# Kernel tuning notes

Hardware: AMD Instinct MI355X
Metric: run time of the kernel (lower is better)

## Reference

```python
import jax, jax.numpy as jnp
import numpy as np

B, P, K, L, F, KS, NCLS = 8, 4096, 20, 10, 32, 5, 40
N = B * P


def setup_inputs() -> dict:
    key = jax.random.key(0)
    k = jax.random.split(key, 5)
    return {
        "pos": jax.random.normal(k[0], (N, 3), jnp.float32),
        "Wsp": jax.random.normal(k[1], (KS ** 3, F), jnp.float32) * 0.1,
        "root": jax.random.normal(k[2], (F,), jnp.float32) * 0.1,
        "bias": jnp.zeros((F,), jnp.float32),
        "gamma": jnp.ones((F,), jnp.float32),
        "beta": jnp.zeros((F,), jnp.float32),
        "W1": jax.random.normal(k[3], (F, 256), jnp.float32) * 0.1,
        "b1": jnp.zeros((256,), jnp.float32),
        "W2": jax.random.normal(k[4], (256, NCLS), jnp.float32) * 0.1,
        "b2": jnp.zeros((NCLS,), jnp.float32),
    }


def _knn(pos):
    # per-graph brute-force knn (loop=False), neighbors sorted by distance
    pts = pos.reshape(B, P, 3)

    def one(p):
        d = jnp.sum((p[:, None, :] - p[None, :, :]) ** 2, -1)  # (P,P)
        d = d.at[jnp.arange(P), jnp.arange(P)].set(jnp.inf)
        return jax.lax.top_k(-d, K)[1]

    nbr = jax.vmap(one)(pts) + (jnp.arange(B) * P)[:, None, None]
    return nbr.reshape(N, K)


def _eig3(A):
    # power iteration with deflation (nr_iterations=5) on batched 3x3 symmetric mats
    def pi(M):
        v = jnp.full((M.shape[0], 3), np.float32(3.0 ** -0.5))
        for _ in range(5):
            v = jnp.einsum("nij,nj->ni", M, v)
            v = v / (jnp.linalg.norm(v, axis=-1, keepdims=True) + 1e-12)
        lam = jnp.einsum("ni,nij,nj->n", v, M, v)
        return lam, v

    l1, v1 = pi(A)
    _, v2 = pi(A - l1[:, None, None] * v1[:, :, None] * v1[:, None, :])
    v3 = jnp.cross(v1, v2)
    v3 = v3 / (jnp.linalg.norm(v3, axis=-1, keepdims=True) + 1e-12)
    return jnp.stack([v1, v2, v3], axis=1)  # rows = eigenvectors, V[:,2] = normal


def reference(pos, Wsp, root, bias, gamma, beta, W1, b1, W2, b2):
    nbr = _knn(pos)                               # (N,K)
    clusters = pos[nbr] - pos[:, None, :]         # (N,K,3) neighbor - center
    cov = jnp.einsum("nmc,nmd->ncd", clusters[:, :L], clusters[:, :L])
    V = _eig3(cov)                                # (N,3,3)
    dirc = jnp.einsum("nkc,ndc->nkd", clusters, V)  # clusters @ V^T
    signs = jnp.sign(dirc[:, :, 2].sum(1))
    dirc = dirc.at[:, :, 2].multiply(signs[:, None])
    max_abs = jnp.max(jnp.abs(dirc).reshape(N, -1), 1)
    dirc = dirc / max_abs[:, None, None] * 0.5 + 0.5  # pseudo coords in [0,1]

    # SplineConv, degree=1, open splines, dim=3, in_channels=1 (x=ones)
    v = dirc * (KS - 1)
    f = jnp.floor(v)
    frac = v - f
    fi = f.astype(jnp.int32)
    bits = jnp.array([[(s >> 2) & 1, (s >> 1) & 1, s & 1] for s in range(8)], jnp.int32)
    idx = jnp.clip(fi[:, :, None, :] + bits[None, None, :, :], 0, KS - 1)  # (N,K,8,3)
    wgt = jnp.where(bits[None, None] == 1, frac[:, :, None, :], 1.0 - frac[:, :, None, :])
    basis = wgt.prod(-1)                                          # (N,K,8)
    flat = (idx[..., 0] * KS + idx[..., 1]) * KS + idx[..., 2]    # (N,K,8)
    msg = jnp.einsum("nks,nksf->nf", basis, Wsp[flat]) / K        # mean aggregation
    node = msg + root + bias                                      # root weight on x=1

    # BatchNorm1d (training-mode batch stats, eps=1e-5)
    mu = node.mean(0)
    var = ((node - mu) ** 2).mean(0)
    xb = gamma * (node - mu) / jnp.sqrt(var + 1e-5) + beta

    out3 = xb[:, :, None] * V[:, 2][:, None, :]   # (N,F,3) scale normal direction
    y = jax.nn.sigmoid(out3)
    ys = y.reshape(-1, P, F).mean(1)              # (3B,F) as in torch .view
    y1 = jax.nn.elu(ys @ W1 + b1)
    return jax.nn.log_softmax(y1 @ W2 + b2, axis=1)
```

## Files before the change

### kernel.cpp

```cpp
#include <hip/hip_runtime.h>
#include <hip/hip_bf16.h>
#include <math.h>

#define BGR 8
#define PP 4096
#define NPTS 32768
#define KNN 20
#define LCOV 10
#define FF 32
#define KS 5
#define NCLS 40
#define NGROUP 24
#define GROUPLEN 131072

#define SPLIT 8
#define CHUNK (PP / SPLIT)
#define PTSBLK 128
#define KTHR 1024
#define NSLOT (KNN + 1)
#define MPAD NSLOT
#define SENT 0xFFFFFFFFu
#define SCELLS 4096
#define SCAP 12

__device__ inline unsigned umn(unsigned a, unsigned b) { return a < b ? a : b; }
__device__ inline unsigned umx(unsigned a, unsigned b) { return a > b ? a : b; }

__device__ inline void mat3vec(const float M[9], const float v[3], float w[3]) {
    w[0] = M[0] * v[0] + M[1] * v[1] + M[2] * v[2];
    w[1] = M[3] * v[0] + M[4] * v[1] + M[5] * v[2];
    w[2] = M[6] * v[0] + M[7] * v[1] + M[8] * v[2];
}

__device__ inline float pi3(const float M[9], float v[3]) {
    v[0] = v[1] = v[2] = 0.57735026918962576f;
#pragma unroll
    for (int it = 0; it < 5; ++it) {
        float w[3];
        mat3vec(M, v, w);
        float nrm = sqrtf(w[0] * w[0] + w[1] * w[1] + w[2] * w[2]) + 1e-12f;
        v[0] = w[0] / nrm;
        v[1] = w[1] / nrm;
        v[2] = w[2] / nrm;
    }
    float w[3];
    mat3vec(M, v, w);
    return v[0] * w[0] + v[1] * w[1] + v[2] * w[2];
}

__global__ __launch_bounds__(KTHR, 4) void knn_kernel(
    const float* __restrict__ pos, unsigned short* __restrict__ nbr16,
    float* __restrict__ Rbuf, float* __restrict__ v3out) {
    __shared__ float smem[4 * PP];
    __shared__ unsigned short mOrig[PP];
    __shared__ unsigned samp[PTSBLK * 24];
    __shared__ float Tseed[PTSBLK];
    __shared__ unsigned scr[KTHR / 64][SCAP][64];
    float* tx = smem;
    float* ty = smem + PP;
    float* tz = smem + 2 * PP;
    float* tw = smem + 3 * PP;
    unsigned short* lnbr = (unsigned short*)(smem + 3 * PP + 2816);

    int b = blockIdx.x >> 5;
    int blkInGraph = blockIdx.x & 31;
    const float* gp = pos + (size_t)b * PP * 3;
    int tid = threadIdx.x;
    int lane = tid & 63;
    int wid = tid >> 6;

    {
        unsigned* cnt = (unsigned*)smem;
        unsigned short* cellOf = (unsigned short*)(smem + 4096);
        unsigned* tsum = (unsigned*)(smem + 6144);
        for (int i = tid; i < SCELLS; i += KTHR) cnt[i] = 0u;
        __syncthreads();
        for (int i = tid; i < PP; i += KTHR) {
            float x = gp[i * 3 + 0];
            float y = gp[i * 3 + 1];
            float z = gp[i * 3 + 2];
            int cx = min(max((int)floorf((x + 4.0f) * 2.0f), 0), 15);
            int cy = min(max((int)floorf((y + 4.0f) * 2.0f), 0), 15);
            int cz = min(max((int)floorf((z + 4.0f) * 2.0f), 0), 15);
            unsigned m = 0;
#pragma unroll
            for (int bb = 0; bb < 4; ++bb)
                m |= (((unsigned)(cx >> bb) & 1u) << (3 * bb + 2)) |
                     (((unsigned)(cy >> bb) & 1u) << (3 * bb + 1)) |
                     (((unsigned)(cz >> bb) & 1u) << (3 * bb + 0));
            cellOf[i] = (unsigned short)m;
            atomicAdd(&cnt[m], 1u);
        }
        __syncthreads();
        unsigned c0 = cnt[4 * tid + 0];
        unsigned c1 = cnt[4 * tid + 1];
        unsigned c2 = cnt[4 * tid + 2];
        unsigned c3 = cnt[4 * tid + 3];
        unsigned local = c0 + c1 + c2 + c3;
        tsum[tid] = local;
        __syncthreads();
        for (int off = 1; off < 1024; off <<= 1) {
            unsigned v = (tid >= off) ? tsum[tid - off] : 0u;
            __syncthreads();
            tsum[tid] += v;
            __syncthreads();
        }
        unsigned base = tsum[tid] - local;
        cnt[4 * tid + 0] = base;
        cnt[4 * tid + 1] = base + c0;
        cnt[4 * tid + 2] = base + c0 + c1;
        cnt[4 * tid + 3] = base + c0 + c1 + c2;
        __syncthreads();
        for (int i = tid; i < PP; i += KTHR) {
            unsigned dst = atomicAdd(&cnt[cellOf[i]], 1u);
            mOrig[dst] = (unsigned short)i;
        }
    }
    __syncthreads();

    for (int i = tid; i < PP; i += KTHR) {
        float x = gp[i * 3 + 0];
        float y = gp[i * 3 + 1];
        float z = gp[i * 3 + 2];
        tx[i] = -2.0f * x;
        ty[i] = -2.0f * y;
        tz[i] = -2.0f * z;
        tw[i] = x * x + y * y + z * z;
    }
    __syncthreads();

    int eighth = tid >> 7;
    int pt = tid & (PTSBLK - 1);
    int qSlot = blkInGraph * PTSBLK + pt;
    int li = mOrig[qSlot];
    float px = -0.5f * tx[li];
    float py = -0.5f * ty[li];
    float pz = -0.5f * tz[li];
    float p2 = tw[li];
    int jbeg = eighth * CHUNK;

    {
        unsigned s0 = SENT, s1 = SENT, s2 = SENT;
#pragma unroll 4
        for (int c = 0; c < 32; ++c) {
            int base = jbeg + c * 16;
            float4 xv = *(const float4*)(tx + base);
            float4 yv = *(const float4*)(ty + base);
            float4 zv = *(const float4*)(tz + base);
            float4 wv = *(const float4*)(tw + base);
            float xa[4] = {xv.x, xv.y, xv.z, xv.w};
            float ya[4] = {yv.x, yv.y, yv.z, yv.w};
            float za[4] = {zv.x, zv.y, zv.z, zv.w};
            float wa[4] = {wv.x, wv.y, wv.z, wv.w};
#pragma unroll
            for (int u = 0; u < 4; ++u) {
                float dh = fmaf(px, xa[u], fmaf(py, ya[u], fmaf(pz, za[u], wa[u])));
                float d = fmaxf(dh + p2, 0.0f);
                unsigned key = (__float_as_uint(d) & 0xFFFFF000u)
                               | (unsigned)(base + u);
                if (base + u == li) key = SENT;
                unsigned t0 = umn(key, s0); key = umx(key, s0); s0 = t0;
                t0 = umn(key, s1); key = umx(key, s1); s1 = t0;
                s2 = umn(key, s2);
            }
        }
        unsigned* sdst = &samp[pt * 24 + eighth * 3];
        sdst[0] = s0; sdst[1] = s1; sdst[2] = s2;
    }
    __syncthreads();
    if (tid < PTSBLK) {
        unsigned g0 = 0, g1 = 0, g2 = 0, g3 = 0;
        const unsigned* ss = &samp[tid * 24];
#pragma unroll
        for (int i = 0; i < 24; ++i) {
            unsigned k = ss[i], a;
            a = umx(k, g0); k = umn(k, g0); g0 = a;
            a = umx(k, g1); k = umn(k, g1); g1 = a;
            a = umx(k, g2); k = umn(k, g2); g2 = a;
            g3 = umx(k, g3);
        }
        Tseed[tid] = __uint_as_float((g3 & 0xFFFFF000u) + 0x2000u);
    }
    __syncthreads();
    float seed_hat = Tseed[pt] - p2;

    unsigned bd[NSLOT];
#pragma unroll
    for (int k = 0; k < NSLOT; k++) bd[k] = SENT;
    float worst_hat = seed_hat;

    unsigned* scrW = &scr[wid][0][0];
    unsigned cnt = 0;

    auto drain = [&]() {
#pragma unroll
        for (int s = 0; s < SCAP; ++s) {
            if (!__any((int)cnt > s)) break;
            unsigned k = (s < (int)cnt) ? scrW[s * 64 + lane] : SENT;
#pragma unroll
            for (int i = 0; i < NSLOT; i++) {
                unsigned lo = umn(k, bd[i]);
                k = umx(k, bd[i]);
                bd[i] = lo;
            }
        }
        cnt = 0;
        unsigned wb = bd[NSLOT - 1];
        float nw = (wb == SENT) ? INFINITY
                                : __uint_as_float(wb & 0xFFFFF000u) - p2;
        worst_hat = fminf(nw, seed_hat);
    };

    for (int jj = jbeg; jj < jbeg + CHUNK; jj += 8) {
        float4 xv0 = *(const float4*)(tx + jj);
        float4 yv0 = *(const float4*)(ty + jj);
        float4 zv0 = *(const float4*)(tz + jj);
        float4 wv0 = *(const float4*)(tw + jj);
        float4 xv1 = *(const float4*)(tx + jj + 4);
        float4 yv1 = *(const float4*)(ty + jj + 4);
        float4 zv1 = *(const float4*)(tz + jj + 4);
        float4 wv1 = *(const float4*)(tw + jj + 4);
        float xa[8] = {xv0.x, xv0.y, xv0.z, xv0.w, xv1.x, xv1.y, xv1.z, xv1.w};
        float ya[8] = {yv0.x, yv0.y, yv0.z, yv0.w, yv1.x, yv1.y, yv1.z, yv1.w};
        float za[8] = {zv0.x, zv0.y, zv0.z, zv0.w, zv1.x, zv1.y, zv1.z, zv1.w};
        float wa[8] = {wv0.x, wv0.y, wv0.z, wv0.w, wv1.x, wv1.y, wv1.z, wv1.w};
#pragma unroll
        for (int u = 0; u < 8; u++) {
            float dh = fmaf(px, xa[u], fmaf(py, ya[u], fmaf(pz, za[u], wa[u])));
            if (dh < worst_hat) {
                float d = fmaxf(dh + p2, 0.0f);
                scrW[cnt * 64 + lane] = (__float_as_uint(d) & 0xFFFFF000u)
                                        | (unsigned)(jj + u);
                cnt++;
            }
        }
        if (__any(cnt >= 4u)) drain();
    }
    drain();

    __syncthreads();
    unsigned* mk = (unsigned*)smem;
    for (int h = 0; h < 2; h++) {
        if ((pt >> 6) == h) {
            int lpt = pt & 63;
#pragma unroll
            for (int k = 0; k < NSLOT; k++)
                mk[(eighth * 64 + lpt) * MPAD + k] = bd[k];
        }
        __syncthreads();
        if (tid < 64) {
            int p = tid;
            const unsigned* base = &mk[p * MPAD];
            int cur[SPLIT];
#pragma unroll
            for (int q = 0; q < SPLIT; q++) cur[q] = 0;
            int lpt2 = h * 64 + p;
            int gi = b * PP + (int)mOrig[blkInGraph * PTSBLK + lpt2];
#pragma unroll
            for (int t = 0; t < NSLOT; t++) {
                unsigned v[SPLIT];
#pragma unroll
                for (int q = 0; q < SPLIT; q++)
                    v[q] = base[q * 64 * MPAD + cur[q]];
                unsigned m = v[0];
#pragma unroll
                for (int q = 1; q < SPLIT; q++) m = umn(m, v[q]);
                if (t > 0) {
                    int local = (int)(m & 0xFFFu);
                    nbr16[(size_t)gi * KNN + (t - 1)] = (unsigned short)local;
                    lnbr[lpt2 * KNN + (t - 1)] = (unsigned short)local;
                }
#pragma unroll
                for (int q = 0; q < SPLIT; q++) cur[q] += (v[q] == m);
            }
        }
        __syncthreads();
    }

    for (int i = tid; i < PP; i += KTHR) {
        tx[i] = gp[i * 3 + 0];
        ty[i] = gp[i * 3 + 1];
        tz[i] = gp[i * 3 + 2];
    }
    __syncthreads();

    if (tid < PTSBLK) {
        int lp = tid;
        int ng = mOrig[blkInGraph * PTSBLK + lp];
        int n = b * PP + ng;
        float qx = tx[ng], qy = ty[ng], qz = tz[ng];
        const unsigned short* ln = &lnbr[lp * KNN];

        float m00 = 0.f, m01 = 0.f, m02 = 0.f, m11 = 0.f, m12 = 0.f, m22 = 0.f;
#pragma unroll
        for (int k = 0; k < LCOV; k++) {
            int id = ln[k];
            float cx = tx[id] - qx;
            float cy = ty[id] - qy;
            float cz = tz[id] - qz;
            m00 += cx * cx; m01 += cx * cy; m02 += cx * cz;
            m11 += cy * cy; m12 += cy * cz; m22 += cz * cz;
        }
        float M[9] = {m00, m01, m02, m01, m11, m12, m02, m12, m22};

        float v1[3], v2[3], v3[3];
        float l1 = pi3(M, v1);
        float M2[9];
#pragma unroll
        for (int c = 0; c < 3; c++)
#pragma unroll
            for (int d = 0; d < 3; d++)
                M2[c * 3 + d] = M[c * 3 + d] - l1 * v1[c] * v1[d];
        pi3(M2, v2);
        v3[0] = v1[1] * v2[2] - v1[2] * v2[1];
        v3[1] = v1[2] * v2[0] - v1[0] * v2[2];
        v3[2] = v1[0] * v2[1] - v1[1] * v2[0];
        {
            float nrm = sqrtf(v3[0] * v3[0] + v3[1] * v3[1] + v3[2] * v3[2]) + 1e-12f;
            v3[0] /= nrm; v3[1] /= nrm; v3[2] /= nrm;
        }

        float ssum = 0.f, mx = 0.f;
#pragma unroll
        for (int k = 0; k < KNN; k++) {
            int id = ln[k];
            float cx = tx[id] - qx;
            float cy = ty[id] - qy;
            float cz = tz[id] - qz;
            float d0 = cx * v1[0] + cy * v1[1] + cz * v1[2];
            float d1 = cx * v2[0] + cy * v2[1] + cz * v2[2];
            float d2 = cx * v3[0] + cy * v3[1] + cz * v3[2];
            ssum += d2;
            mx = fmaxf(mx, fabsf(d0));
            mx = fmaxf(mx, fabsf(d1));
            mx = fmaxf(mx, fabsf(d2));
        }
        float sgn = (ssum > 0.f) ? 1.f : ((ssum < 0.f) ? -1.f : 0.f);

        float sc = 2.0f / mx;
        float* R = Rbuf + (size_t)n * 12;
        R[0] = v1[0] * sc;  R[1] = v1[1] * sc;  R[2] = v1[2] * sc;
        R[3] = v2[0] * sc;  R[4] = v2[1] * sc;  R[5] = v2[2] * sc;
        float s2 = sgn * sc;
        R[6] = v3[0] * s2;  R[7] = v3[1] * s2;  R[8] = v3[2] * s2;
        R[9] = 0.f; R[10] = 0.f; R[11] = 0.f;

        v3out[n * 3 + 0] = v3[0];
        v3out[n * 3 + 1] = v3[1];
        v3out[n * 3 + 2] = v3[2];
    }
}

#define NPB 16
#define SPLBLKS (NPTS / NPB)
__global__ __launch_bounds__(512) void spline_kernel(
    const float* __restrict__ pos, const unsigned short* __restrict__ nbr16,
    const float* __restrict__ Rbuf, const float* __restrict__ Wsp,
    const float* __restrict__ root, const float* __restrict__ bias,
    float* __restrict__ node, float* __restrict__ sums_part) {
    __shared__ float wbuf[NPB * KNN * 8];

    int tid = threadIdx.x;
    if (tid < NPB * KNN) {
        int pt = tid / KNN;
        int k = tid - pt * KNN;
        int n = blockIdx.x * NPB + pt;
        const float4* Rv = (const float4*)(Rbuf + (size_t)n * 12);
        float4 r0 = Rv[0], r1 = Rv[1], r2 = Rv[2];
        float px = pos[n * 3 + 0], py = pos[n * 3 + 1], pz = pos[n * 3 + 2];
        int id = (n & ~(PP - 1)) | (int)nbr16[(size_t)n * KNN + k];
        float cxx = pos[id * 3 + 0] - px;
        float cyy = pos[id * 3 + 1] - py;
        float czz = pos[id * 3 + 2] - pz;
        float v0 = fmaf(cxx, r0.x, fmaf(cyy, r0.y, fmaf(czz, r0.z, 2.0f)));
        float v1 = fmaf(cxx, r0.w, fmaf(cyy, r1.x, fmaf(czz, r1.y, 2.0f)));
        float v2 = fmaf(cxx, r1.z, fmaf(cyy, r1.w, fmaf(czz, r2.x, 2.0f)));
        float f0 = floorf(v0), f1 = floorf(v1), f2 = floorf(v2);
        float fr0 = v0 - f0, fr1 = v1 - f1, fr2 = v2 - f2;
        int fi0 = (int)f0, fi1 = (int)f1, fi2 = (int)f2;
        float* wdst = &wbuf[(pt * KNN + k) * 8];
#pragma unroll
        for (int s = 0; s < 8; s++) {
            int b0 = (s >> 2) & 1, b1 = (s >> 1) & 1, b2s = s & 1;
            int i0 = min(max(fi0 + b0, 0), KS - 1);
            int i1 = min(max(fi1 + b1, 0), KS - 1);
            int i2 = min(max(fi2 + b2s, 0), KS - 1);
            float w = (b0 ? fr0 : 1.f - fr0) * (b1 ? fr1 : 1.f - fr1) *
                      (b2s ? fr2 : 1.f - fr2);
            unsigned flat = (unsigned)((i0 * KS + i1) * KS + i2);
            wdst[s] = __uint_as_float((__float_as_uint(w) & ~127u) | flat);
        }
    }
    __syncthreads();

    int pt = tid >> 5;
    int f = tid & 31;
    const float* wrow = &wbuf[pt * (KNN * 8)];
    float acc = 0.f;
#pragma unroll
    for (int k = 0; k < KNN; k++) {
        float4 wa = *(const float4*)&wrow[k * 8];
        float4 wb = *(const float4*)&wrow[k * 8 + 4];
        float wv[8] = {wa.x, wa.y, wa.z, wa.w, wb.x, wb.y, wb.z, wb.w};
#pragma unroll
        for (int s = 0; s < 8; s++) {
            unsigned u = __float_as_uint(wv[s]) & 127u;
            acc = fmaf(wv[s], Wsp[u * FF + f], acc);
        }
    }
    int n = blockIdx.x * NPB + pt;
    float val = acc * (1.0f / KNN) + root[f] + bias[f];
    node[(size_t)n * FF + f] = val;

    __syncthreads();
    wbuf[tid] = val;
    wbuf[512 + tid] = val * val;
    __syncthreads();
    if (tid < 64) {
        int ff = tid & 31;
        int off = (tid >> 5) * 512;
        float s = 0.f;
#pragma unroll
        for (int p = 0; p < NPB; p++) s += wbuf[off + p * 32 + ff];
        sums_part[(size_t)blockIdx.x * 64 + tid] = s;
    }
}

__global__ __launch_bounds__(256) void stats_kernel(
    const float* __restrict__ sums_part, float* __restrict__ sums_accum) {
    int c = blockIdx.x;
    __shared__ float red[256];
    float s = 0.f;
    for (int r = threadIdx.x; r < SPLBLKS; r += 256)
        s += sums_part[(size_t)r * 64 + c];
    red[threadIdx.x] = s;
    __syncthreads();
    for (int off = 128; off > 0; off >>= 1) {
        if (threadIdx.x < off) red[threadIdx.x] += red[threadIdx.x + off];
        __syncthreads();
    }
    if (threadIdx.x == 0) sums_accum[c] = red[0];
}

#define YSPLIT 32
#define YCHUNK (GROUPLEN / YSPLIT)
__global__ __launch_bounds__(256) void ys_kernel(
    const float* __restrict__ node, const float* __restrict__ v3,
    const float* __restrict__ sums_accum, const float* __restrict__ gamma,
    const float* __restrict__ beta, float* __restrict__ ys_part) {
    __shared__ float sa[FF], sb[FF];
    if (threadIdx.x < FF) {
        int f = threadIdx.x;
        float mu = sums_accum[f] * (1.0f / NPTS);
        float var = sums_accum[FF + f] * (1.0f / NPTS) - mu * mu;
        float inv = 1.0f / sqrtf(var + 1e-5f);
        sa[f] = gamma[f] * inv;
        sb[f] = beta[f] - gamma[f] * inv * mu;
    }
    __syncthreads();

    int g = blockIdx.x >> 5;
    int sub = blockIdx.x & 31;
    int t0 = g * GROUPLEN + sub * YCHUNK + threadIdx.x;
    int n = t0 / 96;
    int r0 = t0 - n * 96;
    int rj[3], fj[3], cj[3], dj[3];
    rj[0] = r0;
    rj[1] = (r0 + 64) % 96;
    rj[2] = (r0 + 32) % 96;
#pragma unroll
    for (int j = 0; j < 3; j++) {
        fj[j] = rj[j] / 3;
        cj[j] = rj[j] - fj[j] * 3;
        dj[j] = (rj[j] >= 32) ? 3 : 2;
    }
    float Sa0 = sa[fj[0]], Sb0 = sb[fj[0]];
    float Sa1 = sa[fj[1]], Sb1 = sb[fj[1]];
    float Sa2 = sa[fj[2]], Sb2 = sb[fj[2]];
    int nf = n * FF;
    int n3 = n * 3;

    float acc = 0.f;
#pragma unroll 1
    for (int tr = 0; tr < 5; tr++) {
        {
            float xb = fmaf(Sa0, node[nf + fj[0]], Sb0);
            float val = xb * v3[n3 + cj[0]];
            acc += 1.0f / (1.0f + __expf(-val));
            nf += dj[0] * FF; n3 += dj[0] * 3;
        }
        {
            float xb = fmaf(Sa1, node[nf + fj[1]], Sb1);
            float val = xb * v3[n3 + cj[1]];
            acc += 1.0f / (1.0f + __expf(-val));
            nf += dj[1] * FF; n3 += dj[1] * 3;
        }
        {
            float xb = fmaf(Sa2, node[nf + fj[2]], Sb2);
            float val = xb * v3[n3 + cj[2]];
            acc += 1.0f / (1.0f + __expf(-val));
            nf += dj[2] * FF; n3 += dj[2] * 3;
        }
    }
    {
        float xb = fmaf(Sa0, node[nf + fj[0]], Sb0);
        float val = xb * v3[n3 + cj[0]];
        acc += 1.0f / (1.0f + __expf(-val));
    }

    __shared__ float red[256];
    red[threadIdx.x] = acc;
    __syncthreads();
    if (threadIdx.x < FF) {
        float s = 0.f;
        for (int t = threadIdx.x; t < 256; t += FF) s += red[t];
        ys_part[(sub * NGROUP + g) * FF + threadIdx.x] = s * (1.0f / PP);
    }
}

__global__ __launch_bounds__(256) void head_kernel(
    const float* __restrict__ ys_part, const float* __restrict__ W1,
    const float* __restrict__ b1, const float* __restrict__ W2,
    const float* __restrict__ b2, float* __restrict__ out) {
    int g = blockIdx.x;
    __shared__ float syr[FF];
    __shared__ float h[256];
    __shared__ float logits[NCLS];
    __shared__ float mstat[2];
    if (threadIdx.x < FF) {
        float s = 0.f;
#pragma unroll
        for (int sub = 0; sub < YSPLIT; sub++)
            s += ys_part[(sub * NGROUP + g) * FF + threadIdx.x];
        syr[threadIdx.x] = s;
    }
    __syncthreads();
    int j = threadIdx.x;
    float acc = b1[j];
#pragma unroll
    for (int f = 0; f < FF; f++) acc += syr[f] * W1[f * 256 + j];
    h[j] = acc > 0.f ? acc : expm1f(acc);
    __syncthreads();
    if (j < NCLS) {
        float l = b2[j];
        for (int q = 0; q < 256; q++) l += h[q] * W2[q * NCLS + j];
        logits[j] = l;
    }
    __syncthreads();
    if (j == 0) {
        float m = -INFINITY;
        for (int o = 0; o < NCLS; o++) m = fmaxf(m, logits[o]);
        float s = 0.f;
        for (int o = 0; o < NCLS; o++) s += expf(logits[o] - m);
        mstat[0] = m;
        mstat[1] = logf(s);
    }
    __syncthreads();
    if (j < NCLS) out[g * NCLS + j] = logits[j] - mstat[0] - mstat[1];
}

extern "C" void kernel_launch(void* const* d_in, const int* in_sizes, int n_in,
                              void* d_out, int out_size, void* d_ws, size_t ws_size,
                              hipStream_t stream) {
    const float* pos   = (const float*)d_in[0];
    const float* Wsp   = (const float*)d_in[1];
    const float* root  = (const float*)d_in[2];
    const float* bias  = (const float*)d_in[3];
    const float* gamma = (const float*)d_in[4];
    const float* beta  = (const float*)d_in[5];
    const float* W1    = (const float*)d_in[6];
    const float* b1    = (const float*)d_in[7];
    const float* W2    = (const float*)d_in[8];
    const float* b2    = (const float*)d_in[9];
    float* out = (float*)d_out;

    char* ws = (char*)d_ws;
    unsigned short* nbr16 = (unsigned short*)(ws);
    float* sums_part = (float*)(ws + 1310720);
    float* ys_part   = (float*)(ws + 1835008);
    float* sums_accum = (float*)(ws + 1933312);
    float* node = (float*)(ws + 2621440);
    float* v3   = (float*)(ws + 6815744);
    float* Rbuf = (float*)(ws + 7212288);

    knn_kernel<<<256, KTHR, 0, stream>>>(pos, nbr16, Rbuf, v3);
    spline_kernel<<<SPLBLKS, 512, 0, stream>>>(pos, nbr16, Rbuf, Wsp, root,
                                               bias, node, sums_part);
    stats_kernel<<<64, 256, 0, stream>>>(sums_part, sums_accum);
    ys_kernel<<<NGROUP * YSPLIT, 256, 0, stream>>>(node, v3, sums_accum, gamma,
                                                   beta, ys_part);
    head_kernel<<<NGROUP, 256, 0, stream>>>(ys_part, W1, b1, W2, b2, out);
}
```

Baseline: 192.8 us.

## Fuse spline convolution and partial batch-norm sums into the knn kernel

Moves the spline basis computation, the Wsp gather-accumulate and the per-block BN partial sums into the end of knn_kernel. Neighbor indices and rotation rows stay in shared memory (lnbr, samp, scr), so the nbr16 and Rbuf global round trips and one launch go away. The cost is that the spline work now runs on only 256 large blocks instead of 2048 small ones, which reduces parallelism for that phase and adds extra barriers and shared-memory reuse inside the already heavy knn kernel.

```diff
diff --git a/kernel.cpp b/kernel.cpp
--- a/kernel.cpp
+++ b/kernel.cpp
@@ -22,6 +22,7 @@
 #define SENT 0xFFFFFFFFu
 #define SCELLS 4096
 #define SCAP 12
+#define KBLKS 256
 
 __device__ inline unsigned umn(unsigned a, unsigned b) { return a < b ? a : b; }
 __device__ inline unsigned umx(unsigned a, unsigned b) { return a > b ? a : b; }
@@ -49,8 +50,10 @@
 }
 
 __global__ __launch_bounds__(KTHR, 4) void knn_kernel(
-    const float* __restrict__ pos, unsigned short* __restrict__ nbr16,
-    float* __restrict__ Rbuf, float* __restrict__ v3out) {
+    const float* __restrict__ pos, const float* __restrict__ Wsp,
+    const float* __restrict__ root, const float* __restrict__ bias,
+    float* __restrict__ node, float* __restrict__ sums_part,
+    float* __restrict__ v3out) {
     __shared__ float smem[4 * PP];
     __shared__ unsigned short mOrig[PP];
     __shared__ unsigned samp[PTSBLK * 24];
@@ -255,7 +258,6 @@
 #pragma unroll
             for (int q = 0; q < SPLIT; q++) cur[q] = 0;
             int lpt2 = h * 64 + p;
-            int gi = b * PP + (int)mOrig[blkInGraph * PTSBLK + lpt2];
 #pragma unroll
             for (int t = 0; t < NSLOT; t++) {
                 unsigned v[SPLIT];
@@ -266,9 +268,7 @@
 #pragma unroll
                 for (int q = 1; q < SPLIT; q++) m = umn(m, v[q]);
                 if (t > 0) {
-                    int local = (int)(m & 0xFFFu);
-                    nbr16[(size_t)gi * KNN + (t - 1)] = (unsigned short)local;
-                    lnbr[lpt2 * KNN + (t - 1)] = (unsigned short)local;
+                    lnbr[lpt2 * KNN + (t - 1)] = (unsigned short)(m & 0xFFFu);
                 }
 #pragma unroll
                 for (int q = 0; q < SPLIT; q++) cur[q] += (v[q] == m);
@@ -338,91 +338,91 @@
         float sgn = (ssum > 0.f) ? 1.f : ((ssum < 0.f) ? -1.f : 0.f);
 
         float sc = 2.0f / mx;
-        float* R = Rbuf + (size_t)n * 12;
-        R[0] = v1[0] * sc;  R[1] = v1[1] * sc;  R[2] = v1[2] * sc;
-        R[3] = v2[0] * sc;  R[4] = v2[1] * sc;  R[5] = v2[2] * sc;
-        float s2 = sgn * sc;
-        R[6] = v3[0] * s2;  R[7] = v3[1] * s2;  R[8] = v3[2] * s2;
-        R[9] = 0.f; R[10] = 0.f; R[11] = 0.f;
+        float* rrow = (float*)samp + lp * 12;
+        rrow[0] = v1[0] * sc;  rrow[1] = v1[1] * sc;  rrow[2] = v1[2] * sc;
+        rrow[3] = v2[0] * sc;  rrow[4] = v2[1] * sc;  rrow[5] = v2[2] * sc;
+        float s2g = sgn * sc;
+        rrow[6] = v3[0] * s2g; rrow[7] = v3[1] * s2g; rrow[8] = v3[2] * s2g;
 
         v3out[n * 3 + 0] = v3[0];
         v3out[n * 3 + 1] = v3[1];
         v3out[n * 3 + 2] = v3[2];
     }
-}
-
-#define NPB 16
-#define SPLBLKS (NPTS / NPB)
-__global__ __launch_bounds__(512) void spline_kernel(
-    const float* __restrict__ pos, const unsigned short* __restrict__ nbr16,
-    const float* __restrict__ Rbuf, const float* __restrict__ Wsp,
-    const float* __restrict__ root, const float* __restrict__ bias,
-    float* __restrict__ node, float* __restrict__ sums_part) {
-    __shared__ float wbuf[NPB * KNN * 8];
-
-    int tid = threadIdx.x;
-    if (tid < NPB * KNN) {
-        int pt = tid / KNN;
-        int k = tid - pt * KNN;
-        int n = blockIdx.x * NPB + pt;
-        const float4* Rv = (const float4*)(Rbuf + (size_t)n * 12);
-        float4 r0 = Rv[0], r1 = Rv[1], r2 = Rv[2];
-        float px = pos[n * 3 + 0], py = pos[n * 3 + 1], pz = pos[n * 3 + 2];
-        int id = (n & ~(PP - 1)) | (int)nbr16[(size_t)n * KNN + k];
-        float cxx = pos[id * 3 + 0] - px;
-        float cyy = pos[id * 3 + 1] - py;
-        float czz = pos[id * 3 + 2] - pz;
-        float v0 = fmaf(cxx, r0.x, fmaf(cyy, r0.y, fmaf(czz, r0.z, 2.0f)));
-        float v1 = fmaf(cxx, r0.w, fmaf(cyy, r1.x, fmaf(czz, r1.y, 2.0f)));
-        float v2 = fmaf(cxx, r1.z, fmaf(cyy, r1.w, fmaf(czz, r2.x, 2.0f)));
-        float f0 = floorf(v0), f1 = floorf(v1), f2 = floorf(v2);
-        float fr0 = v0 - f0, fr1 = v1 - f1, fr2 = v2 - f2;
-        int fi0 = (int)f0, fi1 = (int)f1, fi2 = (int)f2;
-        float* wdst = &wbuf[(pt * KNN + k) * 8];
-#pragma unroll
-        for (int s = 0; s < 8; s++) {
-            int b0 = (s >> 2) & 1, b1 = (s >> 1) & 1, b2s = s & 1;
-            int i0 = min(max(fi0 + b0, 0), KS - 1);
-            int i1 = min(max(fi1 + b1, 0), KS - 1);
-            int i2 = min(max(fi2 + b2s, 0), KS - 1);
-            float w = (b0 ? fr0 : 1.f - fr0) * (b1 ? fr1 : 1.f - fr1) *
-                      (b2s ? fr2 : 1.f - fr2);
-            unsigned flat = (unsigned)((i0 * KS + i1) * KS + i2);
-            wdst[s] = __uint_as_float((__float_as_uint(w) & ~127u) | flat);
-        }
-    }
-    __syncthreads();
-
-    int pt = tid >> 5;
-    int f = tid & 31;
-    const float* wrow = &wbuf[pt * (KNN * 8)];
-    float acc = 0.f;
-#pragma unroll
-    for (int k = 0; k < KNN; k++) {
-        float4 wa = *(const float4*)&wrow[k * 8];
-        float4 wb = *(const float4*)&wrow[k * 8 + 4];
-        float wv[8] = {wa.x, wa.y, wa.z, wa.w, wb.x, wb.y, wb.z, wb.w};
-#pragma unroll
-        for (int s = 0; s < 8; s++) {
-            unsigned u = __float_as_uint(wv[s]) & 127u;
-            acc = fmaf(wv[s], Wsp[u * FF + f], acc);
-        }
-    }
-    int n = blockIdx.x * NPB + pt;
-    float val = acc * (1.0f / KNN) + root[f] + bias[f];
-    node[(size_t)n * FF + f] = val;
-
-    __syncthreads();
-    wbuf[tid] = val;
-    wbuf[512 + tid] = val * val;
-    __syncthreads();
-    if (tid < 64) {
-        int ff = tid & 31;
-        int off = (tid >> 5) * 512;
-        float s = 0.f;
-#pragma unroll
-        for (int p = 0; p < NPB; p++) s += wbuf[off + p * 32 + ff];
-        sums_part[(size_t)blockIdx.x * 64 + tid] = s;
+    __syncthreads();
+
+    {
+        float* wb = (float*)scr;
+        const float* sampF = (const float*)samp;
+        for (int i = tid; i < PTSBLK * KNN; i += KTHR) {
+            int lp = i / KNN;
+            int k = i - lp * KNN;
+            int ng = mOrig[blkInGraph * PTSBLK + lp];
+            float qx = tx[ng], qy = ty[ng], qz = tz[ng];
+            int id = lnbr[lp * KNN + k];
+            float cxx = tx[id] - qx;
+            float cyy = ty[id] - qy;
+            float czz = tz[id] - qz;
+            const float* r = &sampF[lp * 12];
+            float v0 = fmaf(cxx, r[0], fmaf(cyy, r[1], fmaf(czz, r[2], 2.0f)));
+            float v1 = fmaf(cxx, r[3], fmaf(cyy, r[4], fmaf(czz, r[5], 2.0f)));
+            float v2 = fmaf(cxx, r[6], fmaf(cyy, r[7], fmaf(czz, r[8], 2.0f)));
+            float f0 = floorf(v0), f1 = floorf(v1), f2 = floorf(v2);
+            float fr0 = v0 - f0, fr1 = v1 - f1, fr2 = v2 - f2;
+            int fi0 = (int)f0, fi1 = (int)f1, fi2 = (int)f2;
+            float* wdst = &wb[i * 8];
+#pragma unroll
+            for (int s = 0; s < 8; s++) {
+                int b0 = (s >> 2) & 1, b1 = (s >> 1) & 1, b2s = s & 1;
+                int i0 = min(max(fi0 + b0, 0), KS - 1);
+                int i1 = min(max(fi1 + b1, 0), KS - 1);
+                int i2 = min(max(fi2 + b2s, 0), KS - 1);
+                float w = (b0 ? fr0 : 1.f - fr0) * (b1 ? fr1 : 1.f - fr1) *
+                          (b2s ? fr2 : 1.f - fr2);
+                unsigned flat = (unsigned)((i0 * KS + i1) * KS + i2);
+                wdst[s] = __uint_as_float((__float_as_uint(w) & ~127u) | flat);
+            }
+        }
+    }
+    __syncthreads();
+
+    {
+        const float* wb = (const float*)scr;
+        float bn1 = 0.f, bn2 = 0.f;
+        int f = tid & 31;
+#pragma unroll
+        for (int it = 0; it < 4; ++it) {
+            int lp = (tid >> 5) + 32 * it;
+            const float* wrow = &wb[(lp * KNN) * 8];
+            float acc = 0.f;
+#pragma unroll
+            for (int k = 0; k < KNN; k++) {
+                float4 wa = *(const float4*)&wrow[k * 8];
+                float4 wb4 = *(const float4*)&wrow[k * 8 + 4];
+                float wv[8] = {wa.x, wa.y, wa.z, wa.w, wb4.x, wb4.y, wb4.z, wb4.w};
+#pragma unroll
+                for (int s = 0; s < 8; s++) {
+                    unsigned u = __float_as_uint(wv[s]) & 127u;
+                    acc = fmaf(wv[s], Wsp[u * FF + f], acc);
+                }
+            }
+            float val = acc * (1.0f / KNN) + root[f] + bias[f];
+            int ng = mOrig[blkInGraph * PTSBLK + lp];
+            node[((size_t)b * PP + ng) * FF + f] = val;
+            bn1 += val;
+            bn2 += val * val;
+        }
+        float* redF = (float*)samp;
+        redF[tid] = bn1;
+        redF[1024 + tid] = bn2;
+        __syncthreads();
+        if (tid < 64) {
+            int ff = tid & 31;
+            int off = (tid >> 5) * 1024;
+            float s = 0.f;
+#pragma unroll
+            for (int g = 0; g < 32; ++g) s += redF[off + (g << 5) + ff];
+            sums_part[(size_t)blockIdx.x * 64 + tid] = s;
+        }
     }
 }
 
@@ -431,7 +431,7 @@
     int c = blockIdx.x;
     __shared__ float red[256];
     float s = 0.f;
-    for (int r = threadIdx.x; r < SPLBLKS; r += 256)
+    for (int r = threadIdx.x; r < KBLKS; r += 256)
         s += sums_part[(size_t)r * 64 + c];
     red[threadIdx.x] = s;
     __syncthreads();
@@ -575,17 +575,14 @@
     float* out = (float*)d_out;
 
     char* ws = (char*)d_ws;
-    unsigned short* nbr16 = (unsigned short*)(ws);
     float* sums_part = (float*)(ws + 1310720);
     float* ys_part   = (float*)(ws + 1835008);
     float* sums_accum = (float*)(ws + 1933312);
     float* node = (float*)(ws + 2621440);
     float* v3   = (float*)(ws + 6815744);
-    float* Rbuf = (float*)(ws + 7212288);
-
-    knn_kernel<<<256, KTHR, 0, stream>>>(pos, nbr16, Rbuf, v3);
-    spline_kernel<<<SPLBLKS, 512, 0, stream>>>(pos, nbr16, Rbuf, Wsp, root,
-                                               bias, node, sums_part);
+
+    knn_kernel<<<KBLKS, KTHR, 0, stream>>>(pos, Wsp, root, bias, node,
+                                           sums_part, v3);
     stats_kernel<<<64, 256, 0, stream>>>(sums_part, sums_accum);
     ys_kernel<<<NGROUP * YSPLIT, 256, 0, stream>>>(node, v3, sums_accum, gamma,
                                                    beta, ys_part);
```

New measurement: 187.6 us. -2.7%, faster.
